# Kernel tuning notes

Hardware: AMD Instinct MI355X
Metric: run time of the kernel (lower is better)

Reference implementation:

```python
import jax, jax.numpy as jnp
import numpy as np

B, S, D, H = 32, 4096, 128, 8

def setup_inputs() -> dict:
    key = jax.random.key(0)
    kx, kkq, kv = jax.random.split(key, 3)
    x = jax.random.normal(kx, (B, S, D), dtype=jnp.float32)
    # nn.Linear weights: y = x @ W.T, weight shape [D, D]; stacked over heads.
    W_kq = jax.random.normal(kkq, (H, D, D), dtype=jnp.float32)
    W_v = jax.random.normal(kv, (H, D, D), dtype=jnp.float32)
    return {"x": x, "W_kq": W_kq, "W_v": W_v}


def reference(x, W_kq, W_v):
    # Original per-head math:
    #   kq_h = x @ W_kq[h].T                      [B,S,D]
    #   scores_h = x @ kq_h^T = x @ W_kq[h] @ x^T [B,S,S]
    #   out_h = scores_h @ (x @ W_v[h].T)
    # Reassociated (identical math, linear in S):
    #   out = x @ (sum_h W_kq[h] @ (x^T x) @ W_v[h].T)
    G = jnp.einsum('bsd,bse->bde', x, x)              # [B,D,D] = x^T x
    M = jnp.einsum('hde,bef,hgf->bdg', W_kq, G, W_v)  # sum over heads h
    out = jnp.einsum('bsd,bdg->bsg', x, M)            # [B,S,D]
    return out
```

## Files before the change

### kernel.cpp

```cpp
#include <hip/hip_runtime.h>
#include <hip/hip_bf16.h>

#define BB 32
#define SS 4096
#define DD 128
#define HH 8

typedef __attribute__((ext_vector_type(8))) short short8;
typedef __attribute__((ext_vector_type(4))) float f32x4;
typedef unsigned long long u64;

__device__ inline unsigned short f2b(float f){
  unsigned int u = __float_as_uint(f);
  return (unsigned short)((u + 0x7fffu + ((u >> 16) & 1u)) >> 16);
}

__device__ inline int swzi(int r, int c){
  return (r << 7) | (((c >> 3) ^ (r & 7)) << 3) | (c & 7);
}

__device__ inline short8 ldfrag(const short* buf, int row, int kblk){
  return *reinterpret_cast<const short8*>(&buf[(row << 7) | ((kblk ^ (row & 7)) << 3)]);
}

__device__ inline void wave_gemm32x64(const short* bufA, const short* bufB,
                                      int wm, int wn, int lane, f32x4 acc[2][4]){
  #pragma unroll
  for (int ks = 0; ks < 4; ++ks){
    int kblk = ks * 4 + (lane >> 4);
    short8 af[2], bf[4];
    #pragma unroll
    for (int mt = 0; mt < 2; ++mt) af[mt] = ldfrag(bufA, wm + mt * 16 + (lane & 15), kblk);
    #pragma unroll
    for (int nt = 0; nt < 4; ++nt) bf[nt] = ldfrag(bufB, wn + nt * 16 + (lane & 15), kblk);
    #pragma unroll
    for (int mt = 0; mt < 2; ++mt)
      #pragma unroll
      for (int nt = 0; nt < 4; ++nt)
        acc[mt][nt] = __builtin_amdgcn_mfma_f32_16x16x32_bf16(af[mt], bf[nt], acc[mt][nt], 0, 0, 0);
  }
}

__device__ inline u64 packb4(float a, float b, float c, float d){
  return (u64)f2b(a) | ((u64)f2b(b) << 16) | ((u64)f2b(c) << 32) | ((u64)f2b(d) << 48);
}

template<int NT>
__device__ inline void stage128(const float* __restrict__ src, short* dst, int t){
  const float4* s4 = reinterpret_cast<const float4*>(src);
  #pragma unroll
  for (int f4 = t; f4 < 4096; f4 += NT){
    int r = f4 >> 5, c = (f4 & 31) << 2;
    float4 v = s4[f4];
    *reinterpret_cast<u64*>(&dst[swzi(r, c)]) = packb4(v.x, v.y, v.z, v.w);
  }
}

__device__ inline void ld128(const float* __restrict__ src, int t, float4 r[8]){
  const float4* s4 = reinterpret_cast<const float4*>(src);
  #pragma unroll
  for (int i = 0; i < 8; ++i) r[i] = s4[t + i * 512];
}
__device__ inline void wr128(short* dst, int t, const float4 r[8]){
  #pragma unroll
  for (int i = 0; i < 8; ++i){
    int f4 = t + i * 512;
    int rr = f4 >> 5, c = (f4 & 31) << 2;
    *reinterpret_cast<u64*>(&dst[swzi(rr, c)]) = packb4(r[i].x, r[i].y, r[i].z, r[i].w);
  }
}

__global__ __launch_bounds__(512) void k_gram(const float* __restrict__ x, float* __restrict__ Gp){
  __shared__ short xsT[128 * 128];
  const int t = threadIdx.x, lane = t & 63, wid = t >> 6;
  const int slot = blockIdx.x, b = blockIdx.y;
  const int e = t & 127, sg = t >> 7;
  const int wm = (wid >> 1) * 32, wn = (wid & 1) * 64;

  f32x4 acc[2][4];
  const f32x4 z = {0.f, 0.f, 0.f, 0.f};
  #pragma unroll
  for (int i = 0; i < 2; ++i)
    #pragma unroll
    for (int j = 0; j < 4; ++j) acc[i][j] = z;

  const float* xb = x + ((size_t)b * SS + slot * 512) * DD;
  float r0[16], r1[16];
  #pragma unroll
  for (int i = 0; i < 16; ++i){
    int s2 = sg + 4 * i;
    r0[i] = xb[(2 * s2) * DD + e];
    r1[i] = xb[(2 * s2 + 1) * DD + e];
  }
  for (int c = 0; c < 4; ++c){
    __syncthreads();
    #pragma unroll
    for (int i = 0; i < 16; ++i){
      int s2 = sg + 4 * i;
      unsigned int w = (unsigned)f2b(r0[i]) | ((unsigned)f2b(r1[i]) << 16);
      *reinterpret_cast<unsigned int*>(&xsT[swzi(e, 2 * s2)]) = w;
    }
    if (c < 3){
      const float* src = xb + (size_t)(c + 1) * 128 * DD;
      #pragma unroll
      for (int i = 0; i < 16; ++i){
        int s2 = sg + 4 * i;
        r0[i] = src[(2 * s2) * DD + e];
        r1[i] = src[(2 * s2 + 1) * DD + e];
      }
    }
    __syncthreads();
    wave_gemm32x64(xsT, xsT, wm, wn, lane, acc);
  }

  float* Gb = Gp + (size_t)(slot * BB + b) * (DD * DD);
  #pragma unroll
  for (int mt = 0; mt < 2; ++mt)
    #pragma unroll
    for (int nt = 0; nt < 4; ++nt)
      #pragma unroll
      for (int i = 0; i < 4; ++i){
        int ee = wm + mt * 16 + ((lane >> 4) << 2) + i;
        int ff = wn + nt * 16 + (lane & 15);
        Gb[(ee << 7) + ff] = acc[mt][nt][i];
      }
}

__global__ __launch_bounds__(512) void k_heads(const float* __restrict__ Gp,
                                               const float* __restrict__ Wkq,
                                               const float* __restrict__ Wv,
                                               float* __restrict__ Mp){
  __shared__ short bufW[128 * 128];
  __shared__ short bufG[128 * 128];
  __shared__ short bufT[128 * 128];
  const int t = threadIdx.x, lane = t & 63, wid = t >> 6;
  const int h = blockIdx.x, b = blockIdx.y;
  const int wm = (wid >> 1) * 32, wn = (wid & 1) * 64;
  const f32x4 z = {0.f, 0.f, 0.f, 0.f};

  stage128<512>(Wv + (size_t)h * DD * DD, bufW, t);
  {
    const float4* g4 = reinterpret_cast<const float4*>(Gp);
    #pragma unroll
    for (int it = 0; it < 8; ++it){
      int f4 = t + it * 512;
      float4 s = {0.f, 0.f, 0.f, 0.f};
      #pragma unroll
      for (int sl = 0; sl < 8; ++sl){
        float4 v = g4[(size_t)(sl * BB + b) * 4096 + f4];
        s.x += v.x; s.y += v.y; s.z += v.z; s.w += v.w;
      }
      int r = f4 >> 5, c = (f4 & 31) << 2;
      *reinterpret_cast<u64*>(&bufG[swzi(r, c)]) = packb4(s.x, s.y, s.z, s.w);
    }
  }
  __syncthreads();

  float4 wk[8];
  ld128(Wkq + (size_t)h * DD * DD, t, wk);

  f32x4 acc[2][4];
  #pragma unroll
  for (int i = 0; i < 2; ++i)
    #pragma unroll
    for (int j = 0; j < 4; ++j) acc[i][j] = z;
  wave_gemm32x64(bufW, bufG, wm, wn, lane, acc);
  __syncthreads();

  #pragma unroll
  for (int mt = 0; mt < 2; ++mt)
    #pragma unroll
    for (int nt = 0; nt < 4; ++nt)
      #pragma unroll
      for (int i = 0; i < 4; ++i){
        int g = wm + mt * 16 + ((lane >> 4) << 2) + i;
        int e = wn + nt * 16 + (lane & 15);
        bufT[swzi(g, e)] = (short)f2b(acc[mt][nt][i]);
      }
  wr128(bufW, t, wk);
  __syncthreads();

  #pragma unroll
  for (int i = 0; i < 2; ++i)
    #pragma unroll
    for (int j = 0; j < 4; ++j) acc[i][j] = z;
  wave_gemm32x64(bufT, bufW, wm, wn, lane, acc);

  float* Mb = Mp + (size_t)(h * BB + b) * (DD * DD);
  #pragma unroll
  for (int mt = 0; mt < 2; ++mt)
    #pragma unroll
    for (int nt = 0; nt < 4; ++nt)
      #pragma unroll
      for (int i = 0; i < 4; ++i){
        int g = wm + mt * 16 + ((lane >> 4) << 2) + i;
        int d = wn + nt * 16 + (lane & 15);
        Mb[(g << 7) + d] = acc[mt][nt][i];
      }
}

__global__ __launch_bounds__(256) void k_red(const float* __restrict__ Mp, short* __restrict__ Mb){
  const int id = blockIdx.x * 256 + threadIdx.x;
  const float4* p4 = reinterpret_cast<const float4*>(Mp);
  u64* o8 = reinterpret_cast<u64*>(Mb);
  #pragma unroll
  for (int it = 0; it < 4; ++it){
    int F = id + it * 32768;
    int b = F >> 12, j4 = F & 4095;
    float4 s = {0.f, 0.f, 0.f, 0.f};
    #pragma unroll
    for (int hh = 0; hh < 8; ++hh){
      float4 v = p4[(size_t)(hh * BB + b) * 4096 + j4];
      s.x += v.x; s.y += v.y; s.z += v.z; s.w += v.w;
    }
    o8[F] = packb4(s.x, s.y, s.z, s.w);
  }
}

__global__ __launch_bounds__(512) void k_out(const float* __restrict__ x,
                                             const short* __restrict__ Mbf,
                                             float* __restrict__ out){
  __shared__ short bufM[128 * 128];
  __shared__ short bufX[128 * 128];
  const int t = threadIdx.x, lane = t & 63, wid = t >> 6;
  const int b = blockIdx.y, s0 = blockIdx.x * 256;
  const int wm = (wid >> 1) * 32, wn = (wid & 1) * 64;
  const f32x4 z = {0.f, 0.f, 0.f, 0.f};

  {
    const short8* m8 = reinterpret_cast<const short8*>(Mbf + (size_t)b * DD * DD);
    #pragma unroll
    for (int i = 0; i < 4; ++i){
      int idx = t + i * 512;
      int r = idx >> 4, c8 = idx & 15;
      *reinterpret_cast<short8*>(&bufM[(r << 7) | ((c8 ^ (r & 7)) << 3)]) = m8[idx];
    }
  }
  const float* xb = x + ((size_t)b * SS + s0) * DD;
  float4 xr[8];
  ld128(xb, t, xr);

  for (int c = 0; c < 2; ++c){
    __syncthreads();
    wr128(bufX, t, xr);
    if (c < 1) ld128(xb + (size_t)128 * DD, t, xr);
    __syncthreads();

    f32x4 acc[2][4];
    #pragma unroll
    for (int i = 0; i < 2; ++i)
      #pragma unroll
      for (int j = 0; j < 4; ++j) acc[i][j] = z;
    wave_gemm32x64(bufX, bufM, wm, wn, lane, acc);

    float* ob = out + ((size_t)b * SS + s0 + c * 128) * DD;
    #pragma unroll
    for (int mt = 0; mt < 2; ++mt)
      #pragma unroll
      for (int nt = 0; nt < 4; ++nt)
        #pragma unroll
        for (int i = 0; i < 4; ++i){
          int sp = wm + mt * 16 + ((lane >> 4) << 2) + i;
          int g = wn + nt * 16 + (lane & 15);
          ob[(sp << 7) + g] = acc[mt][nt][i];
        }
  }
}

extern "C" void kernel_launch(void* const* d_in, const int* in_sizes, int n_in,
                              void* d_out, int out_size, void* d_ws, size_t ws_size,
                              hipStream_t stream) {
  const float* x   = (const float*)d_in[0];
  const float* Wkq = (const float*)d_in[1];
  const float* Wv  = (const float*)d_in[2];
  float* out = (float*)d_out;

  float* Gp = (float*)d_ws;
  float* Mp = Gp + (size_t)8 * BB * DD * DD;
  short* Mb = (short*)(Mp + (size_t)HH * BB * DD * DD);

  k_gram <<<dim3(8, BB),       512, 0, stream>>>(x, Gp);
  k_heads<<<dim3(HH, BB),      512, 0, stream>>>(Gp, Wkq, Wv, Mp);
  k_red  <<<dim3(128),         256, 0, stream>>>(Mp, Mb);
  k_out  <<<dim3(SS / 256, BB), 512, 0, stream>>>(x, Mb, out);
}
```

Baseline: 159.8 us.

## Pre-reduce Gram partials once and load x fragments directly from global in k_out

Adds a separate k_gsum kernel that sums the 8 Gram partial slots once per batch and stores them as swizzled bf16, so the 8 k_heads blocks per batch no longer each redo that 8-way fp32 reduction. k_out drops its LDS staging of x and instead loads MFMA A-fragments straight from global memory, converting them to bf16 in registers, which removes two barriers per chunk and halves LDS use. The cost is an extra kernel launch, and x fragment loads that are less coalesced and repeated by the two wave columns, possibly raising global memory traffic in the largest kernel.

```diff
diff --git a/kernel.cpp b/kernel.cpp
--- a/kernel.cpp
+++ b/kernel.cpp
@@ -21,6 +21,15 @@
 
 __device__ inline short8 ldfrag(const short* buf, int row, int kblk){
   return *reinterpret_cast<const short8*>(&buf[(row << 7) | ((kblk ^ (row & 7)) << 3)]);
+}
+
+__device__ inline short8 ldxfrag(const float* __restrict__ base, int row, int kblk){
+  const float4* p = reinterpret_cast<const float4*>(base) + row * 32 + kblk * 2;
+  float4 a = p[0], b = p[1];
+  short8 r;
+  r[0] = (short)f2b(a.x); r[1] = (short)f2b(a.y); r[2] = (short)f2b(a.z); r[3] = (short)f2b(a.w);
+  r[4] = (short)f2b(b.x); r[5] = (short)f2b(b.y); r[6] = (short)f2b(b.z); r[7] = (short)f2b(b.w);
+  return r;
 }
 
 __device__ inline void wave_gemm32x64(const short* bufA, const short* bufB,
@@ -126,7 +135,25 @@
       }
 }
 
-__global__ __launch_bounds__(512) void k_heads(const float* __restrict__ Gp,
+__global__ __launch_bounds__(256) void k_gsum(const float* __restrict__ Gp, short* __restrict__ Gbf){
+  const int id = blockIdx.x * 256 + threadIdx.x;
+  const float4* g4 = reinterpret_cast<const float4*>(Gp);
+  #pragma unroll
+  for (int it = 0; it < 4; ++it){
+    int F = id + it * 32768;
+    int b = F >> 12, j4 = F & 4095;
+    float4 s = {0.f, 0.f, 0.f, 0.f};
+    #pragma unroll
+    for (int sl = 0; sl < 8; ++sl){
+      float4 v = g4[(size_t)(sl * BB + b) * 4096 + j4];
+      s.x += v.x; s.y += v.y; s.z += v.z; s.w += v.w;
+    }
+    int r = j4 >> 5, c = (j4 & 31) << 2;
+    *reinterpret_cast<u64*>(&Gbf[(size_t)b * 16384 + swzi(r, c)]) = packb4(s.x, s.y, s.z, s.w);
+  }
+}
+
+__global__ __launch_bounds__(512) void k_heads(const short* __restrict__ Gbf,
                                                const float* __restrict__ Wkq,
                                                const float* __restrict__ Wv,
                                                float* __restrict__ Mp){
@@ -140,19 +167,10 @@
 
   stage128<512>(Wv + (size_t)h * DD * DD, bufW, t);
   {
-    const float4* g4 = reinterpret_cast<const float4*>(Gp);
-    #pragma unroll
-    for (int it = 0; it < 8; ++it){
-      int f4 = t + it * 512;
-      float4 s = {0.f, 0.f, 0.f, 0.f};
-      #pragma unroll
-      for (int sl = 0; sl < 8; ++sl){
-        float4 v = g4[(size_t)(sl * BB + b) * 4096 + f4];
-        s.x += v.x; s.y += v.y; s.z += v.z; s.w += v.w;
-      }
-      int r = f4 >> 5, c = (f4 & 31) << 2;
-      *reinterpret_cast<u64*>(&bufG[swzi(r, c)]) = packb4(s.x, s.y, s.z, s.w);
-    }
+    const short8* g8 = reinterpret_cast<const short8*>(Gbf + (size_t)b * 16384);
+    short8* d8 = reinterpret_cast<short8*>(bufG);
+    #pragma unroll
+    for (int i = 0; i < 4; ++i) d8[t + i * 512] = g8[t + i * 512];
   }
   __syncthreads();
 
@@ -221,7 +239,6 @@
                                              const short* __restrict__ Mbf,
                                              float* __restrict__ out){
   __shared__ short bufM[128 * 128];
-  __shared__ short bufX[128 * 128];
   const int t = threadIdx.x, lane = t & 63, wid = t >> 6;
   const int b = blockIdx.y, s0 = blockIdx.x * 256;
   const int wm = (wid >> 1) * 32, wn = (wid & 1) * 64;
@@ -236,22 +253,32 @@
       *reinterpret_cast<short8*>(&bufM[(r << 7) | ((c8 ^ (r & 7)) << 3)]) = m8[idx];
     }
   }
+  __syncthreads();
+
   const float* xb = x + ((size_t)b * SS + s0) * DD;
-  float4 xr[8];
-  ld128(xb, t, xr);
-
+  #pragma unroll
   for (int c = 0; c < 2; ++c){
-    __syncthreads();
-    wr128(bufX, t, xr);
-    if (c < 1) ld128(xb + (size_t)128 * DD, t, xr);
-    __syncthreads();
-
     f32x4 acc[2][4];
     #pragma unroll
     for (int i = 0; i < 2; ++i)
       #pragma unroll
       for (int j = 0; j < 4; ++j) acc[i][j] = z;
-    wave_gemm32x64(bufX, bufM, wm, wn, lane, acc);
+
+    #pragma unroll
+    for (int ks = 0; ks < 4; ++ks){
+      int kblk = ks * 4 + (lane >> 4);
+      short8 af[2], bf[4];
+      #pragma unroll
+      for (int mt = 0; mt < 2; ++mt)
+        af[mt] = ldxfrag(xb, c * 128 + wm + mt * 16 + (lane & 15), kblk);
+      #pragma unroll
+      for (int nt = 0; nt < 4; ++nt) bf[nt] = ldfrag(bufM, wn + nt * 16 + (lane & 15), kblk);
+      #pragma unroll
+      for (int mt = 0; mt < 2; ++mt)
+        #pragma unroll
+        for (int nt = 0; nt < 4; ++nt)
+          acc[mt][nt] = __builtin_amdgcn_mfma_f32_16x16x32_bf16(af[mt], bf[nt], acc[mt][nt], 0, 0, 0);
+    }
 
     float* ob = out + ((size_t)b * SS + s0 + c * 128) * DD;
     #pragma unroll
@@ -275,12 +302,14 @@
   const float* Wv  = (const float*)d_in[2];
   float* out = (float*)d_out;
 
-  float* Gp = (float*)d_ws;
-  float* Mp = Gp + (size_t)8 * BB * DD * DD;
-  short* Mb = (short*)(Mp + (size_t)HH * BB * DD * DD);
-
-  k_gram <<<dim3(8, BB),       512, 0, stream>>>(x, Gp);
-  k_heads<<<dim3(HH, BB),      512, 0, stream>>>(Gp, Wkq, Wv, Mp);
-  k_red  <<<dim3(128),         256, 0, stream>>>(Mp, Mb);
+  float* Gp  = (float*)d_ws;
+  float* Mp  = Gp + (size_t)8 * BB * DD * DD;
+  short* Gbf = (short*)(Mp + (size_t)HH * BB * DD * DD);
+  short* Mb  = Gbf + (size_t)BB * DD * DD;
+
+  k_gram <<<dim3(8, BB),        512, 0, stream>>>(x, Gp);
+  k_gsum <<<dim3(128),          256, 0, stream>>>(Gp, Gbf);
+  k_heads<<<dim3(HH, BB),       512, 0, stream>>>(Gbf, Wkq, Wv, Mp);
+  k_red  <<<dim3(128),          256, 0, stream>>>(Mp, Mb);
   k_out  <<<dim3(SS / 256, BB), 512, 0, stream>>>(x, Mb, out);
 }
```

After: 152.2 us. 4.8% less time.
